# Kernel tuning notes

Measured on AMD Instinct MI355X. Metric: run time of the kernel, lower is better.

The kernel has to match this reference:

```python
import jax, jax.numpy as jnp
import numpy as np

N, E, H, G, C = 50000, 800000, 512, 64, 2
BERT = 768


def setup_inputs() -> dict:
    key = jax.random.key(0)
    ks = jax.random.split(key, 12)
    sem = jax.random.normal(ks[0], (N, BERT), jnp.float32)
    mask = jax.random.randint(ks[1], (N, 1), 0, 2).astype(jnp.float32)
    x = jnp.concatenate([sem, mask], axis=1)  # [N, 769]
    edge_index = jax.random.randint(ks[2], (2, E), 0, N)
    batch = jnp.sort(jax.random.randint(ks[3], (N,), 0, G))
    s = lambda k, shp, fan: jax.random.normal(k, shp, jnp.float32) / np.float32(np.sqrt(fan))
    return dict(
        x=x, edge_index=edge_index, batch=batch,
        sem_W=s(ks[4], (BERT, H), BERT), sem_b=jnp.zeros((H,), jnp.float32),
        slice_emb=jax.random.normal(ks[5], (2, H), jnp.float32),
        ln_g=jnp.ones((H,), jnp.float32), ln_b=jnp.zeros((H,), jnp.float32),
        conv1_W=s(ks[6], (H, H), H), conv1_b=jnp.zeros((H,), jnp.float32),
        conv2_W=s(ks[7], (H, H), H), conv2_b=jnp.zeros((H,), jnp.float32),
        cls_W1=s(ks[8], (H, H), H), cls_b1=jnp.zeros((H,), jnp.float32),
        cls_W2=s(ks[9], (H, C), H), cls_b2=jnp.zeros((C,), jnp.float32),
    )


def _layer_norm(x, g, b, eps=1e-5):
    m = x.mean(-1, keepdims=True)
    v = x.var(-1, keepdims=True)
    return (x - m) * jax.lax.rsqrt(v + eps) * g + b


def _gcn_conv(h, src, dst, W, b):
    # PyG GCNConv: add self-loops, sym-normalized aggregation of X @ W, plus bias
    hw = h @ W  # [N, H]
    deg = jnp.zeros((N,), hw.dtype).at[dst].add(1.0) + 1.0  # +1 self-loop
    dinv = jax.lax.rsqrt(deg)
    coef = dinv[src] * dinv[dst]  # [E]
    agg = jax.ops.segment_sum(hw[src] * coef[:, None], dst, num_segments=N)
    agg = agg + hw * (dinv * dinv)[:, None]  # self-loop contribution
    return agg + b


def reference(x, edge_index, batch, sem_W, sem_b, slice_emb, ln_g, ln_b,
              conv1_W, conv1_b, conv2_W, conv2_b, cls_W1, cls_b1, cls_W2, cls_b2):
    sem = x[:, :BERT]
    idx = x[:, BERT].astype(jnp.int32)  # binary slice mask
    h = sem @ sem_W + sem_b + slice_emb[idx]
    h = jax.nn.gelu(_layer_norm(h, ln_g, ln_b), approximate=False)
    src, dst = edge_index[0], edge_index[1]
    h = jax.nn.gelu(_gcn_conv(h, src, dst, conv1_W, conv1_b), approximate=False)
    h2 = jax.nn.gelu(_gcn_conv(h, src, dst, conv2_W, conv2_b), approximate=False)
    h = h + h2  # residual (args.residual=True)
    sums = jax.ops.segment_sum(h, batch, num_segments=G)
    cnt = jax.ops.segment_sum(jnp.ones((N,), h.dtype), batch, num_segments=G)
    hg = sums / jnp.maximum(cnt, 1.0)[:, None]  # global mean pool [G, H]
    z = jax.nn.gelu(hg @ cls_W1 + cls_b1, approximate=False)
    return z @ cls_W2 + cls_b2  # [G, C]
```

## Files before the change

### kernel.cpp

```cpp
#include <hip/hip_runtime.h>
#include <hip/hip_bf16.h>

typedef unsigned short u16;
typedef __bf16 bfv8 __attribute__((ext_vector_type(8)));
typedef float f32x4 __attribute__((ext_vector_type(4)));
typedef unsigned int u32x2 __attribute__((ext_vector_type(2)));
typedef unsigned int u32x4 __attribute__((ext_vector_type(4)));

#define HH 512
#define BERT_D 768

__device__ __forceinline__ float gelu_f(float x) {
  return 0.5f * x * (1.0f + erff(x * 0.70710678118654752440f));
}
__device__ __forceinline__ float us2f(u16 u) {
  union { unsigned int i; float f; } c; c.i = ((unsigned int)u) << 16; return c.f;
}
__device__ __forceinline__ u16 f2us(float f) {
  union { float f; unsigned int i; } c; c.f = f;
  unsigned int i = c.i;
  i += 0x7FFFu + ((i >> 16) & 1u);
  return (u16)(i >> 16);
}
__device__ __forceinline__ void gl_lds16(const u16* g, u16* l) {
  __builtin_amdgcn_global_load_lds((const __attribute__((address_space(1))) void*)g,
                                   (__attribute__((address_space(3))) void*)l, 16, 0, 0);
}

__global__ void k_convert_x(const float* __restrict__ x, u16* __restrict__ semb,
                            int* __restrict__ idx, int Nn) {
  const int n = blockIdx.x;
  const int t = threadIdx.x;
  const float* xr = x + (size_t)n * (BERT_D + 1);
  u16* sr = semb + (size_t)n * BERT_D;
#pragma unroll
  for (int i = 0; i < 3; ++i) sr[t + i * 256] = f2us(xr[t + i * 256]);
  if (t == 0) idx[n] = (int)xr[BERT_D];
}

__global__ void k_transpose_bf16(const float* __restrict__ src, u16* __restrict__ dst,
                                 int K, int Nn) {
  int i = blockIdx.x * blockDim.x + threadIdx.x;
  if (i >= K * Nn) return;
  int k = i / Nn, j = i - k * Nn;
  dst[(size_t)j * K + k] = f2us(src[i]);
}

__global__ void k_deg(const int* __restrict__ dst, int* __restrict__ deg, int E) {
  int e = blockIdx.x * blockDim.x + threadIdx.x;
  if (e < E) atomicAdd(&deg[dst[e]], 1);
}

__launch_bounds__(256)
__global__ void k_part(const int* __restrict__ deg, int* __restrict__ part, int Nn) {
  const int i = blockIdx.x * 256 + threadIdx.x;
  int v = (i < Nn) ? deg[i] : 0;
#pragma unroll
  for (int o = 32; o; o >>= 1) v += __shfl_xor(v, o);
  __shared__ int ws4[4];
  if ((threadIdx.x & 63) == 0) ws4[threadIdx.x >> 6] = v;
  __syncthreads();
  if (threadIdx.x == 0) part[blockIdx.x] = ws4[0] + ws4[1] + ws4[2] + ws4[3];
}

__launch_bounds__(256)
__global__ void k_scan_part(int* __restrict__ part, int* __restrict__ row_ptr,
                            int nb, int Nn) {
  __shared__ int sm[256];
  const int t = threadIdx.x;
  int v = (t < nb) ? part[t] : 0;
  sm[t] = v;
  __syncthreads();
  for (int d = 1; d < 256; d <<= 1) {
    int u = (t >= d) ? sm[t - d] : 0;
    __syncthreads();
    sm[t] += u;
    __syncthreads();
  }
  if (t < nb) part[t] = sm[t] - v;
  if (t == 255) row_ptr[Nn] = sm[255];
}

__launch_bounds__(256)
__global__ void k_scan_write(const int* __restrict__ deg, const int* __restrict__ part,
                             int* __restrict__ row_ptr, int* __restrict__ cursor,
                             float* __restrict__ dinv, int Nn) {
  __shared__ int sm[256];
  const int t = threadIdx.x;
  const int i = blockIdx.x * 256 + t;
  int v = (i < Nn) ? deg[i] : 0;
  sm[t] = v;
  __syncthreads();
  for (int d = 1; d < 256; d <<= 1) {
    int u = (t >= d) ? sm[t - d] : 0;
    __syncthreads();
    sm[t] += u;
    __syncthreads();
  }
  if (i < Nn) {
    int pre = part[blockIdx.x] + sm[t] - v;
    row_ptr[i] = pre;
    cursor[i] = pre;
    dinv[i] = rsqrtf((float)v + 1.0f);
  }
}

__global__ void k_csr(const int* __restrict__ src, const int* __restrict__ dst,
                      int* __restrict__ cursor, int* __restrict__ csr_src, int E) {
  int e = blockIdx.x * blockDim.x + threadIdx.x;
  if (e >= E) return;
  int d = dst[e];
  int pos = atomicAdd(&cursor[d], 1);
  csr_src[pos] = src[e];
}

template <int EPI>
__launch_bounds__(256, 2)
__global__ void k_gemm_bt(const u16* __restrict__ A, int lda,
                          const u16* __restrict__ B, int ldb,
                          u16* __restrict__ C, int M, int Kd,
                          const float* __restrict__ bias,
                          const float* __restrict__ emb,
                          const int* __restrict__ idx,
                          const float* __restrict__ dscale) {
  __shared__ alignas(16) u16 As[128 * 64];
  __shared__ alignas(16) u16 Bs[256 * 64];
  const int t = threadIdx.x;
  const int l = t & 63;
  const int w = t >> 6;
  const int wro = (w >> 1) * 64;
  const int wco = (w & 1) * 128;
  const int lr = l & 15;
  const int kg = (l >> 4) * 8;
  const int brow = blockIdx.x * 128;
  const int bcol = blockIdx.y * 256;

  f32x4 acc[4][8] = {};

  for (int k0 = 0; k0 < Kd; k0 += 64) {
#pragma unroll
    for (int i = 0; i < 4; ++i) {
      const int eo = (i * 256 + t) * 8;
      const int r = eo >> 6;
      const int c = eo & 63;
      int gr = brow + r;
      if (gr > M - 1) gr = M - 1;
      gl_lds16(A + (size_t)gr * lda + (k0 + c), As + eo);
    }
#pragma unroll
    for (int i = 0; i < 8; ++i) {
      const int eo = (i * 256 + t) * 8;
      const int r = eo >> 6;
      const int c = eo & 63;
      gl_lds16(B + (size_t)(bcol + r) * ldb + (k0 + c), Bs + eo);
    }
    __syncthreads();
#pragma unroll
    for (int ks = 0; ks < 2; ++ks) {
      bfv8 af[4], bfr[8];
#pragma unroll
      for (int m = 0; m < 4; ++m)
        af[m] = __builtin_bit_cast(bfv8, *(const uint4*)(As + (wro + m * 16 + lr) * 64 + ks * 32 + kg));
#pragma unroll
      for (int n = 0; n < 8; ++n)
        bfr[n] = __builtin_bit_cast(bfv8, *(const uint4*)(Bs + (wco + n * 16 + lr) * 64 + ks * 32 + kg));
#pragma unroll
      for (int m = 0; m < 4; ++m)
#pragma unroll
        for (int n = 0; n < 8; ++n)
          acc[m][n] = __builtin_amdgcn_mfma_f32_16x16x32_bf16(af[m], bfr[n], acc[m][n], 0, 0, 0);
    }
    __syncthreads();
  }

#pragma unroll
  for (int m = 0; m < 4; ++m) {
#pragma unroll
    for (int r = 0; r < 4; ++r) {
      const int row = brow + wro + m * 16 + (l >> 4) * 4 + r;
      if (row >= M) continue;
      const float sc = (EPI == 2) ? dscale[row] : 1.0f;
#pragma unroll
      for (int n = 0; n < 8; ++n) {
        const int col = bcol + wco + n * 16 + lr;
        float v = acc[m][n][r];
        if (EPI == 1) v += bias[col] + emb[idx[row] * HH + col];
        if (EPI == 2) v *= sc;
        C[(size_t)row * HH + col] = f2us(v);
      }
    }
  }
}

__launch_bounds__(256)
__global__ void k_ln_gelu(const u16* __restrict__ h0, const float* __restrict__ gw,
                          const float* __restrict__ bw, u16* __restrict__ hout, int Nn) {
  const int wid = (int)((blockIdx.x * (long long)blockDim.x + threadIdx.x) >> 6);
  if (wid >= Nn) return;
  const int l = threadIdx.x & 63;
  uint4 q = *(const uint4*)(h0 + (size_t)wid * HH + l * 8);
  const u16* us = (const u16*)&q;
  float f[8]; float s = 0.f, s2 = 0.f;
#pragma unroll
  for (int j = 0; j < 8; ++j) { f[j] = us2f(us[j]); s += f[j]; s2 += f[j] * f[j]; }
#pragma unroll
  for (int o = 32; o; o >>= 1) { s += __shfl_xor(s, o); s2 += __shfl_xor(s2, o); }
  const float mean = s * (1.f / 512.f);
  const float var = s2 * (1.f / 512.f) - mean * mean;
  const float rs = rsqrtf(var + 1e-5f);
  union { u16 ov[8]; uint4 q; } o;
#pragma unroll
  for (int j = 0; j < 8; ++j) {
    int col = l * 8 + j;
    float y = (f[j] - mean) * rs * gw[col] + bw[col];
    o.ov[j] = f2us(gelu_f(y));
  }
  *(uint4*)(hout + (size_t)wid * HH + l * 8) = o.q;
}

__launch_bounds__(256)
__global__ void k_agg(const u16* __restrict__ hwS, const int* __restrict__ row_ptr,
                      const int* __restrict__ csr_src, const float* __restrict__ dinv,
                      const float* __restrict__ bias, u16* __restrict__ hout, int Nn) {
  const int wid = (int)((blockIdx.x * (long long)blockDim.x + threadIdx.x) >> 6);
  if (wid >= Nn) return;
  const int l = threadIdx.x & 63;
  const int cb = l * 8;
  float acc[8] = {0.f, 0.f, 0.f, 0.f, 0.f, 0.f, 0.f, 0.f};
  const int lo = row_ptr[wid], hi = row_ptr[wid + 1];
  const float dv = dinv[wid];
  int e = lo;
  for (; e + 4 <= hi; e += 4) {
    const int u0 = csr_src[e + 0];
    const int u1 = csr_src[e + 1];
    const int u2 = csr_src[e + 2];
    const int u3 = csr_src[e + 3];
    uint4 q0 = *(const uint4*)(hwS + (size_t)u0 * HH + cb);
    uint4 q1 = *(const uint4*)(hwS + (size_t)u1 * HH + cb);
    uint4 q2 = *(const uint4*)(hwS + (size_t)u2 * HH + cb);
    uint4 q3 = *(const uint4*)(hwS + (size_t)u3 * HH + cb);
    const u16* p0 = (const u16*)&q0;
    const u16* p1 = (const u16*)&q1;
    const u16* p2 = (const u16*)&q2;
    const u16* p3 = (const u16*)&q3;
#pragma unroll
    for (int j = 0; j < 8; ++j)
      acc[j] += (us2f(p0[j]) + us2f(p1[j])) + (us2f(p2[j]) + us2f(p3[j]));
  }
  for (; e < hi; ++e) {
    const int u = csr_src[e];
    uint4 q = *(const uint4*)(hwS + (size_t)u * HH + cb);
    const u16* p = (const u16*)&q;
#pragma unroll
    for (int j = 0; j < 8; ++j) acc[j] += us2f(p[j]);
  }
  {
    uint4 q = *(const uint4*)(hwS + (size_t)wid * HH + cb);
    const u16* p = (const u16*)&q;
#pragma unroll
    for (int j = 0; j < 8; ++j) acc[j] += us2f(p[j]);
  }
  union { u16 ov[8]; u32x4 q; } o;
#pragma unroll
  for (int j = 0; j < 8; ++j) {
    float v = acc[j] * dv + bias[cb + j];
    o.ov[j] = f2us(gelu_f(v));
  }
  __builtin_nontemporal_store(o.q, (u32x4*)(hout + (size_t)wid * HH + cb));
}

#define POOL_RS 16
__launch_bounds__(256)
__global__ void k_pool2(const u16* __restrict__ h1, const u16* __restrict__ h2,
                        const int* __restrict__ batch, float* __restrict__ hg, int Nn) {
  const int g = blockIdx.x;
  const int chunk = blockIdx.y;
  const int t = threadIdx.x;
  const int w = t >> 6;
  const int l = t & 63;
  const int cb = l * 8;
  int lo, hi;
  { int a = 0, b = Nn; while (a < b) { int m = (a + b) >> 1; if (batch[m] < g) a = m + 1; else b = m; } lo = a; }
  { int a = 0, b = Nn; while (a < b) { int m = (a + b) >> 1; if (batch[m] < g + 1) a = m + 1; else b = m; } hi = a; }
  const int len = hi - lo;
  const int per = (len + POOL_RS - 1) / POOL_RS;
  const int rlo = lo + chunk * per;
  const int rhi = min(rlo + per, hi);
  float acc[8] = {};
  for (int r = rlo + w; r < rhi; r += 4) {
    u32x4 a = __builtin_nontemporal_load((const u32x4*)(h1 + (size_t)r * HH + cb));
    u32x4 b = __builtin_nontemporal_load((const u32x4*)(h2 + (size_t)r * HH + cb));
    const u16* ua = (const u16*)&a;
    const u16* ub = (const u16*)&b;
#pragma unroll
    for (int j = 0; j < 8; ++j) acc[j] += us2f(ua[j]) + us2f(ub[j]);
  }
  __shared__ float red[4][HH];
#pragma unroll
  for (int j = 0; j < 8; ++j) red[w][cb + j] = acc[j];
  __syncthreads();
  if (w == 0) {
#pragma unroll
    for (int j = 0; j < 8; ++j) {
      const int col = cb + j;
      float s = red[0][col] + red[1][col] + red[2][col] + red[3][col];
      if (s != 0.f) atomicAdd(&hg[(size_t)g * HH + col], s);
    }
  }
}

__launch_bounds__(256)
__global__ void k_cls(const float* __restrict__ hg, const int* __restrict__ batch,
                      const float* __restrict__ W1, const float* __restrict__ b1,
                      const float* __restrict__ W2, const float* __restrict__ b2,
                      float* __restrict__ out, int Nn) {
  const int g = blockIdx.x;
  const int t = threadIdx.x;
  __shared__ float hl[512];
  __shared__ float zl[512];
  __shared__ float pr[512];
  int lo, hi;
  { int a = 0, b = Nn; while (a < b) { int m = (a + b) >> 1; if (batch[m] < g) a = m + 1; else b = m; } lo = a; }
  { int a = 0, b = Nn; while (a < b) { int m = (a + b) >> 1; if (batch[m] < g + 1) a = m + 1; else b = m; } hi = a; }
  const float inv = 1.0f / fmaxf((float)(hi - lo), 1.0f);
  hl[t] = hg[(size_t)g * HH + t] * inv;
  hl[t + 256] = hg[(size_t)g * HH + t + 256] * inv;
  __syncthreads();
#pragma unroll
  for (int jj = 0; jj < 2; ++jj) {
    const int j = t + jj * 256;
    float a = b1[j];
    for (int k = 0; k < 512; ++k) a += hl[k] * W1[k * HH + j];
    zl[j] = gelu_f(a);
  }
  __syncthreads();
  float p0 = 0.f, p1 = 0.f;
  for (int k = t; k < 512; k += 256) { p0 += zl[k] * W2[k * 2]; p1 += zl[k] * W2[k * 2 + 1]; }
  pr[t] = p0; pr[t + 256] = p1;
  __syncthreads();
  for (int s2 = 128; s2; s2 >>= 1) {
    if (t < s2) { pr[t] += pr[t + s2]; pr[t + 256] += pr[t + 256 + s2]; }
    __syncthreads();
  }
  if (t == 0) { out[g * 2] = pr[0] + b2[0]; out[g * 2 + 1] = pr[256] + b2[1]; }
}

extern "C" void kernel_launch(void* const* d_in, const int* in_sizes, int n_in,
                              void* d_out, int out_size, void* d_ws, size_t ws_size,
                              hipStream_t stream) {
  const float* x        = (const float*)d_in[0];
  const int*   eidx     = (const int*)d_in[1];
  const int*   batch    = (const int*)d_in[2];
  const float* sem_W    = (const float*)d_in[3];
  const float* sem_b    = (const float*)d_in[4];
  const float* sl_emb   = (const float*)d_in[5];
  const float* ln_g     = (const float*)d_in[6];
  const float* ln_b     = (const float*)d_in[7];
  const float* W1       = (const float*)d_in[8];
  const float* b1       = (const float*)d_in[9];
  const float* W2       = (const float*)d_in[10];
  const float* b2       = (const float*)d_in[11];
  const float* cW1      = (const float*)d_in[12];
  const float* cb1      = (const float*)d_in[13];
  const float* cW2      = (const float*)d_in[14];
  const float* cb2      = (const float*)d_in[15];
  const int N_ = in_sizes[2];
  const int E_ = in_sizes[1] / 2;
  const int G_ = out_size / 2;
  const int* src = eidx;
  const int* dst = eidx + E_;

  char* ws = (char*)d_ws;
  size_t off = 0;
  auto alloc = [&](size_t bytes) -> void* {
    void* p = (void*)(ws + off);
    off += (bytes + 255) & ~(size_t)255;
    return p;
  };
  u16* semb = (u16*)alloc((size_t)N_ * BERT_D * sizeof(u16));
  u16* h1 = semb;
  u16* h0 = (u16*)alloc((size_t)N_ * HH * sizeof(u16));
  u16* hw = h0;
  u16* h = (u16*)alloc((size_t)N_ * HH * sizeof(u16));
  u16* h2 = h;
  u16* semW_T = (u16*)alloc((size_t)HH * BERT_D * sizeof(u16));
  u16* W1T    = (u16*)alloc((size_t)HH * HH * sizeof(u16));
  u16* W2T    = (u16*)alloc((size_t)HH * HH * sizeof(u16));
  int* idx     = (int*)alloc((size_t)N_ * 4);
  int* deg     = (int*)alloc((size_t)N_ * 4);
  float* dinv  = (float*)alloc((size_t)N_ * 4);
  int* row_ptr = (int*)alloc((size_t)(N_ + 1) * 4);
  int* cursor  = (int*)alloc((size_t)N_ * 4);
  int* csr_src = (int*)alloc((size_t)E_ * 4);
  int* part    = (int*)alloc(1024);
  float* hg    = (float*)alloc((size_t)G_ * HH * 4);

  hipMemsetAsync(deg, 0, (size_t)N_ * 4, stream);
  hipMemsetAsync(hg, 0, (size_t)G_ * HH * 4, stream);

  k_convert_x<<<N_, 256, 0, stream>>>(x, semb, idx, N_);
  k_transpose_bf16<<<(BERT_D * HH + 255) / 256, 256, 0, stream>>>(sem_W, semW_T, BERT_D, HH);
  k_transpose_bf16<<<(HH * HH + 255) / 256, 256, 0, stream>>>(W1, W1T, HH, HH);
  k_transpose_bf16<<<(HH * HH + 255) / 256, 256, 0, stream>>>(W2, W2T, HH, HH);

  const int nb = (N_ + 255) / 256;
  k_deg<<<(E_ + 255) / 256, 256, 0, stream>>>(dst, deg, E_);
  k_part<<<nb, 256, 0, stream>>>(deg, part, N_);
  k_scan_part<<<1, 256, 0, stream>>>(part, row_ptr, nb, N_);
  k_scan_write<<<nb, 256, 0, stream>>>(deg, part, row_ptr, cursor, dinv, N_);
  k_csr<<<(E_ + 255) / 256, 256, 0, stream>>>(src, dst, cursor, csr_src, E_);

  const int Mtiles = (N_ + 127) / 128;
  const int wave_blocks = (N_ + 3) / 4;

  k_gemm_bt<1><<<dim3(Mtiles, HH / 256), 256, 0, stream>>>(
      semb, BERT_D, semW_T, BERT_D, h0, N_, BERT_D, sem_b, sl_emb, idx, nullptr);
  k_ln_gelu<<<wave_blocks, 256, 0, stream>>>(h0, ln_g, ln_b, h, N_);
  k_gemm_bt<2><<<dim3(Mtiles, HH / 256), 256, 0, stream>>>(
      h, HH, W1T, HH, hw, N_, HH, nullptr, nullptr, nullptr, dinv);
  k_agg<<<wave_blocks, 256, 0, stream>>>(hw, row_ptr, csr_src, dinv, b1, h1, N_);
  k_gemm_bt<2><<<dim3(Mtiles, HH / 256), 256, 0, stream>>>(
      h1, HH, W2T, HH, hw, N_, HH, nullptr, nullptr, nullptr, dinv);
  k_agg<<<wave_blocks, 256, 0, stream>>>(hw, row_ptr, csr_src, dinv, b2, h2, N_);
  k_pool2<<<dim3(G_, POOL_RS), 256, 0, stream>>>(h1, h2, batch, hg, N_);
  k_cls<<<G_, 256, 0, stream>>>(hg, batch, cW1, cb1, cW2, cb2, (float*)d_out, N_);
}
```

Before: 740.9 us.

## Fuse fp32-to-bf16 input conversion into first GEMM and swizzle GEMM blocks by XCD

```diff
diff --git a/kernel.cpp b/kernel.cpp
--- a/kernel.cpp
+++ b/kernel.cpp
@@ -4,11 +4,11 @@
 typedef unsigned short u16;
 typedef __bf16 bfv8 __attribute__((ext_vector_type(8)));
 typedef float f32x4 __attribute__((ext_vector_type(4)));
-typedef unsigned int u32x2 __attribute__((ext_vector_type(2)));
 typedef unsigned int u32x4 __attribute__((ext_vector_type(4)));
 
 #define HH 512
 #define BERT_D 768
+#define XSTRIDE 769
 
 __device__ __forceinline__ float gelu_f(float x) {
   return 0.5f * x * (1.0f + erff(x * 0.70710678118654752440f));
@@ -27,15 +27,9 @@
                                    (__attribute__((address_space(3))) void*)l, 16, 0, 0);
 }
 
-__global__ void k_convert_x(const float* __restrict__ x, u16* __restrict__ semb,
-                            int* __restrict__ idx, int Nn) {
-  const int n = blockIdx.x;
-  const int t = threadIdx.x;
-  const float* xr = x + (size_t)n * (BERT_D + 1);
-  u16* sr = semb + (size_t)n * BERT_D;
-#pragma unroll
-  for (int i = 0; i < 3; ++i) sr[t + i * 256] = f2us(xr[t + i * 256]);
-  if (t == 0) idx[n] = (int)xr[BERT_D];
+__global__ void k_idx(const float* __restrict__ x, int* __restrict__ idx, int Nn) {
+  int i = blockIdx.x * blockDim.x + threadIdx.x;
+  if (i < Nn) idx[i] = (int)x[(size_t)i * XSTRIDE + BERT_D];
 }
 
 __global__ void k_transpose_bf16(const float* __restrict__ src, u16* __restrict__ dst,
@@ -114,14 +108,94 @@
   csr_src[pos] = src[e];
 }
 
+__launch_bounds__(256, 2)
+__global__ void k_gemm1(const float* __restrict__ xf,
+                        const u16* __restrict__ B, int ldb,
+                        u16* __restrict__ C, int M,
+                        const float* __restrict__ bias,
+                        const float* __restrict__ emb,
+                        const int* __restrict__ idx) {
+  __shared__ alignas(16) u16 As[128 * 64];
+  __shared__ alignas(16) u16 Bs[256 * 64];
+  const int t = threadIdx.x;
+  const int l = t & 63;
+  const int w = t >> 6;
+  const int wro = (w >> 1) * 64;
+  const int wco = (w & 1) * 128;
+  const int lr = l & 15;
+  const int kg = (l >> 4) * 8;
+  const int nwg = gridDim.x;
+  const int id = blockIdx.x;
+  const int q8 = nwg >> 3, r8 = nwg & 7;
+  const int xcd = id & 7, rk = id >> 3;
+  const int swz = (xcd < r8 ? xcd * (q8 + 1) : r8 * (q8 + 1) + (xcd - r8) * q8) + rk;
+  const int brow = (swz >> 1) * 128;
+  const int bcol = (swz & 1) * 256;
+
+  const int arr = t >> 4;
+  const int ac4 = (t & 15) * 4;
+
+  f32x4 acc[4][8] = {};
+
+  for (int k0 = 0; k0 < BERT_D; k0 += 64) {
+#pragma unroll
+    for (int i = 0; i < 8; ++i) {
+      const int eo = (i * 256 + t) * 8;
+      const int r = eo >> 6;
+      const int c = eo & 63;
+      gl_lds16(B + (size_t)(bcol + r) * ldb + (k0 + c), Bs + eo);
+    }
+#pragma unroll
+    for (int i = 0; i < 8; ++i) {
+      const int rr = i * 16 + arr;
+      int gr = brow + rr;
+      if (gr > M - 1) gr = M - 1;
+      const float* xp = xf + (size_t)gr * XSTRIDE + k0 + ac4;
+      float f0 = xp[0], f1 = xp[1], f2 = xp[2], f3 = xp[3];
+      union { u16 h[4]; unsigned long long q; } pk;
+      pk.h[0] = f2us(f0); pk.h[1] = f2us(f1); pk.h[2] = f2us(f2); pk.h[3] = f2us(f3);
+      *(unsigned long long*)(As + rr * 64 + ac4) = pk.q;
+    }
+    __syncthreads();
+#pragma unroll
+    for (int ks = 0; ks < 2; ++ks) {
+      bfv8 af[4], bfr[8];
+#pragma unroll
+      for (int m = 0; m < 4; ++m)
+        af[m] = __builtin_bit_cast(bfv8, *(const uint4*)(As + (wro + m * 16 + lr) * 64 + ks * 32 + kg));
+#pragma unroll
+      for (int n = 0; n < 8; ++n)
+        bfr[n] = __builtin_bit_cast(bfv8, *(const uint4*)(Bs + (wco + n * 16 + lr) * 64 + ks * 32 + kg));
+#pragma unroll
+      for (int m = 0; m < 4; ++m)
+#pragma unroll
+        for (int n = 0; n < 8; ++n)
+          acc[m][n] = __builtin_amdgcn_mfma_f32_16x16x32_bf16(af[m], bfr[n], acc[m][n], 0, 0, 0);
+    }
+    __syncthreads();
+  }
+
+#pragma unroll
+  for (int m = 0; m < 4; ++m) {
+#pragma unroll
+    for (int r = 0; r < 4; ++r) {
+      const int row = brow + wro + m * 16 + (l >> 4) * 4 + r;
+      if (row >= M) continue;
+#pragma unroll
+      for (int n = 0; n < 8; ++n) {
+        const int col = bcol + wco + n * 16 + lr;
+        float v = acc[m][n][r] + bias[col] + emb[idx[row] * HH + col];
+        C[(size_t)row * HH + col] = f2us(v);
+      }
+    }
+  }
+}
+
 template <int EPI>
 __launch_bounds__(256, 2)
 __global__ void k_gemm_bt(const u16* __restrict__ A, int lda,
                           const u16* __restrict__ B, int ldb,
                           u16* __restrict__ C, int M, int Kd,
-                          const float* __restrict__ bias,
-                          const float* __restrict__ emb,
-                          const int* __restrict__ idx,
                           const float* __restrict__ dscale) {
   __shared__ alignas(16) u16 As[128 * 64];
   __shared__ alignas(16) u16 Bs[256 * 64];
@@ -132,8 +206,13 @@
   const int wco = (w & 1) * 128;
   const int lr = l & 15;
   const int kg = (l >> 4) * 8;
-  const int brow = blockIdx.x * 128;
-  const int bcol = blockIdx.y * 256;
+  const int nwg = gridDim.x;
+  const int id = blockIdx.x;
+  const int q8 = nwg >> 3, r8 = nwg & 7;
+  const int xcd = id & 7, rk = id >> 3;
+  const int swz = (xcd < r8 ? xcd * (q8 + 1) : r8 * (q8 + 1) + (xcd - r8) * q8) + rk;
+  const int brow = (swz >> 1) * 128;
+  const int bcol = (swz & 1) * 256;
 
   f32x4 acc[4][8] = {};
 
@@ -184,7 +263,6 @@
       for (int n = 0; n < 8; ++n) {
         const int col = bcol + wco + n * 16 + lr;
         float v = acc[m][n][r];
-        if (EPI == 1) v += bias[col] + emb[idx[row] * HH + col];
         if (EPI == 2) v *= sc;
         C[(size_t)row * HH + col] = f2us(v);
       }
@@ -377,8 +455,7 @@
     off += (bytes + 255) & ~(size_t)255;
     return p;
   };
-  u16* semb = (u16*)alloc((size_t)N_ * BERT_D * sizeof(u16));
-  u16* h1 = semb;
+  u16* h1 = (u16*)alloc((size_t)N_ * HH * sizeof(u16));
   u16* h0 = (u16*)alloc((size_t)N_ * HH * sizeof(u16));
   u16* hw = h0;
   u16* h = (u16*)alloc((size_t)N_ * HH * sizeof(u16));
@@ -398,7 +475,7 @@
   hipMemsetAsync(deg, 0, (size_t)N_ * 4, stream);
   hipMemsetAsync(hg, 0, (size_t)G_ * HH * 4, stream);
 
-  k_convert_x<<<N_, 256, 0, stream>>>(x, semb, idx, N_);
+  k_idx<<<(N_ + 255) / 256, 256, 0, stream>>>(x, idx, N_);
   k_transpose_bf16<<<(BERT_D * HH + 255) / 256, 256, 0, stream>>>(sem_W, semW_T, BERT_D, HH);
   k_transpose_bf16<<<(HH * HH + 255) / 256, 256, 0, stream>>>(W1, W1T, HH, HH);
   k_transpose_bf16<<<(HH * HH + 255) / 256, 256, 0, stream>>>(W2, W2T, HH, HH);
@@ -412,15 +489,16 @@
 
   const int Mtiles = (N_ + 127) / 128;
   const int wave_blocks = (N_ + 3) / 4;
-
-  k_gemm_bt<1><<<dim3(Mtiles, HH / 256), 256, 0, stream>>>(
-      semb, BERT_D, semW_T, BERT_D, h0, N_, BERT_D, sem_b, sl_emb, idx, nullptr);
+  const int gemm_grid = Mtiles * 2;
+
+  k_gemm1<<<gemm_grid, 256, 0, stream>>>(
+      x, semW_T, BERT_D, h0, N_, sem_b, sl_emb, idx);
   k_ln_gelu<<<wave_blocks, 256, 0, stream>>>(h0, ln_g, ln_b, h, N_);
-  k_gemm_bt<2><<<dim3(Mtiles, HH / 256), 256, 0, stream>>>(
-      h, HH, W1T, HH, hw, N_, HH, nullptr, nullptr, nullptr, dinv);
+  k_gemm_bt<2><<<gemm_grid, 256, 0, stream>>>(
+      h, HH, W1T, HH, hw, N_, HH, dinv);
   k_agg<<<wave_blocks, 256, 0, stream>>>(hw, row_ptr, csr_src, dinv, b1, h1, N_);
-  k_gemm_bt<2><<<dim3(Mtiles, HH / 256), 256, 0, stream>>>(
-      h1, HH, W2T, HH, hw, N_, HH, nullptr, nullptr, nullptr, dinv);
+  k_gemm_bt<2><<<gemm_grid, 256, 0, stream>>>(
+      h1, HH, W2T, HH, hw, N_, HH, dinv);
   k_agg<<<wave_blocks, 256, 0, stream>>>(hw, row_ptr, csr_src, dinv, b2, h2, N_);
   k_pool2<<<dim3(G_, POOL_RS), 256, 0, stream>>>(h1, h2, batch, hg, N_);
   k_cls<<<G_, 256, 0, stream>>>(hg, batch, cW1, cb1, cW2, cb2, (float*)d_out, N_);
```

Result: faster. 725.3 us (-2.1%).
